# Kernel tuning notes

Hardware: AMD Instinct MI355X
Metric: run time of the kernel (lower is better)

## Reference

```python
import jax, jax.numpy as jnp
import numpy as np

N_HEAD = 16

def setup_inputs() -> dict:
    key = jax.random.key(0)
    ks = jax.random.split(key, 9)
    H = 2048
    def w(k, shape, scale=0.02):
        return jax.random.normal(k, shape, dtype=jnp.float32) * scale
    return {
        'h':  jax.random.normal(ks[0], (4, 2048, H), dtype=jnp.float32),
        'Wq': w(ks[1], (H, H)), 'bq': w(ks[2], (H,)),
        'Wk': w(ks[3], (H, H)), 'bk': w(ks[4], (H,)),
        'Wv': w(ks[5], (H, H)), 'bv': w(ks[6], (H,)),
        'Wo': w(ks[7], (H, H)), 'bo': w(ks[8], (H,)),
    }

def reference(h, Wq, bq, Wk, bk, Wv, bv, Wo, bo):
    B, S, H = h.shape
    nh = N_HEAD
    hd = H // nh
    # QKV projections (torch Linear: x @ W.T + b)
    q = (h @ Wq.T + bq).reshape(B, S, nh, hd)
    k = (h @ Wk.T + bk).reshape(B, S, nh, hd)
    v = (h @ Wv.T + bv).reshape(B, S, nh, hd)
    scale = 1.0 / jnp.sqrt(jnp.float32(hd))
    # causal attention scores [B, nh, S, S]
    scores = jnp.einsum('bqhd,bkhd->bhqk', q, k) * scale
    causal = jnp.tril(jnp.ones((S, S), dtype=bool))
    scores = jnp.where(causal, scores, jnp.finfo(scores.dtype).min)
    attn = jax.nn.softmax(scores, axis=-1)
    o = jnp.einsum('bhqk,bkhd->bqhd', attn, v).reshape(B, S, H)
    return o @ Wo.T + bo
```

## Files before the change

kernel.cpp:

```cpp
#include <hip/hip_runtime.h>
#include <hip/hip_bf16.h>
#include <math.h>


using bf16x8 = __attribute__((ext_vector_type(8))) __bf16;
using f32x4  = __attribute__((ext_vector_type(4))) float;
using s16x8  = __attribute__((ext_vector_type(8))) short;

#define MFMA16(a, b, c) __builtin_amdgcn_mfma_f32_16x16x32_bf16((a), (b), (c), 0, 0, 0)

__device__ __forceinline__ unsigned short f2bf(float f) {
  unsigned u = __float_as_uint(f);
  u += 0x7FFFu + ((u >> 16) & 1u);
  return (unsigned short)(u >> 16);
}

__device__ __forceinline__ void gload16(const void* g, void* l) {
  __builtin_amdgcn_global_load_lds((const __attribute__((address_space(1))) void*)g,
                                   (__attribute__((address_space(3))) void*)l,
                                   16, 0, 0);
}

__global__ void cvt_kernel(const float* __restrict__ in, unsigned short* __restrict__ out, int n4) {
  int i = blockIdx.x * 256 + threadIdx.x;
  if (i >= n4) return;
  float4 v = ((const float4*)in)[i];
  ushort4 o;
  o.x = f2bf(v.x); o.y = f2bf(v.y); o.z = f2bf(v.z); o.w = f2bf(v.w);
  ((ushort4*)out)[i] = o;
}


#define GEMM_PRE()                                                             \
  const int tid = threadIdx.x;                                                 \
  const int wave = tid >> 6, lane = tid & 63;                                  \
  const int lo = lane & 15, hi = lane >> 4;                                    \
  const int wr = wave >> 2, wc = wave & 3;                                     \
  const int r4 = lane >> 2, s4 = lane & 3;                                     \
  const int scol = ((s4 ^ ((r4 >> 1) & 3)) << 3);                              \
  const unsigned short* aS[2]; const unsigned short* bS[2];                    \
  _Pragma("unroll")                                                            \
  for (int j = 0; j < 2; ++j) {                                                \
    aS[j] = A + (size_t)(m0 + (wave * 2 + j) * 16 + r4) * 2048 + scol;         \
    bS[j] = W + (size_t)(n0 + (wave * 2 + j) * 16 + r4) * 2048 + scol;         \
  }                                                                            \
  f32x4 acc[8][4] = {};

#define STAGE2(BUF, J)                                                         \
  do {                                                                         \
    gload16(aS[J], &lA[BUF][(wave * 2 + (J)) * 512]);                          \
    gload16(bS[J], &lB[BUF][(wave * 2 + (J)) * 512]);                          \
    aS[J] += 32; bS[J] += 32;                                                  \
  } while (0)

#define LDA4_(dst, MH, BUF)                                                    \
  do {                                                                         \
    _Pragma("unroll")                                                          \
    for (int im = 0; im < 4; ++im)                                             \
      dst[im] = *(const bf16x8*)&lA[BUF][(wr * 128 + (MH)*64 + im * 16 + lo) * 32 + \
                                         ((hi ^ ((lo >> 1) & 3)) << 3)];       \
  } while (0)

#define LDB4_(dst, BUF)                                                        \
  do {                                                                         \
    _Pragma("unroll")                                                          \
    for (int ni = 0; ni < 4; ++ni)                                             \
      dst[ni] = *(const bf16x8*)&lB[BUF][(wc * 64 + ni * 16 + lo) * 32 +       \
                                         ((hi ^ ((lo >> 1) & 3)) << 3)];       \
  } while (0)

#define MF16(MH, aF, bF)                                                       \
  do {                                                                         \
    __builtin_amdgcn_s_setprio(1);                                             \
    _Pragma("unroll")                                                          \
    for (int im = 0; im < 4; ++im)                                             \
      _Pragma("unroll")                                                        \
      for (int ni = 0; ni < 4; ++ni)                                           \
        acc[(MH)*4 + im][ni] = MFMA16(aF[im], bF[ni], acc[(MH)*4 + im][ni]);   \
    __builtin_amdgcn_s_setprio(0);                                             \
  } while (0)

#define BAR __builtin_amdgcn_s_barrier()
#define VMC(N) asm volatile("s_waitcnt vmcnt(" #N ")" ::: "memory")

#define TILE(RBUF, SBUF, COND, VN)                                             \
  do {                                                                         \
    bf16x8 aF[4], aG[4], bF[4];                                                \
    LDA4_(aF, 0, RBUF); LDB4_(bF, RBUF);                                       \
    if (COND) STAGE2(SBUF, 0);                                                 \
    BAR; MF16(0, aF, bF); BAR;                                                 \
    LDA4_(aG, 1, RBUF);                                                        \
    if (COND) STAGE2(SBUF, 1);                                                 \
    BAR; MF16(1, aG, bF); VMC(VN); BAR;                                        \
  } while (0)

#define GEMM_MAIN()                                                            \
  STAGE2(0, 0); STAGE2(0, 1); STAGE2(1, 0); STAGE2(1, 1);                      \
  STAGE2(2, 0); STAGE2(2, 1);                                                  \
  VMC(8); BAR;                                                                 \
  for (int u = 0; u < 15; ++u) {                                               \
    TILE(0, 3, true, 8); TILE(1, 0, true, 8);                                  \
    TILE(2, 1, true, 8); TILE(3, 2, true, 8);                                  \
  }                                                                            \
  TILE(0, 3, true, 8); TILE(1, 0, false, 4);                                   \
  TILE(2, 1, false, 0); TILE(3, 2, false, 0);

__global__ __launch_bounds__(512, 2)
void gemm_qkv(const unsigned short* __restrict__ A,
              const unsigned short* __restrict__ W,
              const float* __restrict__ bq, const float* __restrict__ bk,
              const float* __restrict__ bv,
              unsigned short* __restrict__ Q, unsigned short* __restrict__ Kq,
              unsigned short* __restrict__ V) {
  __shared__ unsigned short lA[4][256 * 32];
  __shared__ unsigned short lB[4][256 * 32];
  const int bid = blockIdx.x;
  const int sid = (bid & 7) * 96 + (bid >> 3);
  const int bm = sid / 24, bn = sid % 24;
  const int m0 = bm * 256, n0 = bn * 256;
  GEMM_PRE();
  GEMM_MAIN();

  const int which = n0 >> 11;
  const float* bias = (which == 0) ? bq : (which == 1) ? bk : bv;
  unsigned short* dst = (which == 0) ? Q : (which == 1) ? Kq : V;
#pragma unroll
  for (int mi = 0; mi < 8; mi++)
#pragma unroll
    for (int ni = 0; ni < 4; ni++) {
      int n_g = n0 + wc * 64 + ni * 16 + lo;
      int n2 = n_g & 2047;
      int head = n2 >> 7, d = n2 & 127;
      float bb = bias[n2];
#pragma unroll
      for (int i = 0; i < 4; i++) {
        int m = m0 + wr * 128 + mi * 16 + hi * 4 + i;
        int b = m >> 11, s = m & 2047;
        dst[(((size_t)b * 16 + head) * 2048 + s) * 128 + d] = f2bf(acc[mi][ni][i] + bb);
      }
    }
}

__global__ __launch_bounds__(512, 2)
void gemm_out(const unsigned short* __restrict__ A,
              const unsigned short* __restrict__ W,
              const float* __restrict__ bo, float* __restrict__ out) {
  __shared__ unsigned short lA[4][256 * 32];
  __shared__ unsigned short lB[4][256 * 32];
  const int bid = blockIdx.x;
  const int sid = (bid & 7) * 32 + (bid >> 3);
  const int bm = sid >> 3, bn = sid & 7;
  const int m0 = bm * 256, n0 = bn * 256;
  GEMM_PRE();
  GEMM_MAIN();

#pragma unroll
  for (int mi = 0; mi < 8; mi++)
#pragma unroll
    for (int ni = 0; ni < 4; ni++) {
      int n_g = n0 + wc * 64 + ni * 16 + lo;
      float bb = bo[n_g];
#pragma unroll
      for (int i = 0; i < 4; i++) {
        int m = m0 + wr * 128 + mi * 16 + hi * 4 + i;
        out[(size_t)m * 2048 + n_g] = acc[mi][ni][i] + bb;
      }
    }
}

__global__ __launch_bounds__(256, 2)
void attn_kernel(const unsigned short* __restrict__ Qb,
                 const unsigned short* __restrict__ Kb,
                 const unsigned short* __restrict__ Vb,
                 unsigned short* __restrict__ Ob) {
  __shared__ unsigned short lK[32 * 128];
  __shared__ unsigned short lVt[144 * 42];
  __shared__ unsigned short lP[4][32 * 40];

  const int tid = threadIdx.x;
  const int wave = tid >> 6, lane = tid & 63;
  const int lo = lane & 15, hi = lane >> 4;
  const int bh = blockIdx.x & 63;
  const int qt = 15 - (blockIdx.x >> 6);
  const int q0 = qt * 128 + wave * 32;
  const size_t base = (size_t)bh * 2048 * 128;
  const float SCL = 0.08838834764831845f * 1.4426950408889634f;
  const float THR = 11.5416f;

#pragma unroll
  for (int x = tid; x < 512; x += 256)
    lVt[(128 + (x >> 5)) * 42 + (x & 31)] = 0x3F80;

  bf16x8 aq[2][4];
#pragma unroll
  for (int mi = 0; mi < 2; mi++)
#pragma unroll
    for (int dk = 0; dk < 4; dk++)
      aq[mi][dk] = *(const bf16x8*)&Qb[base + (size_t)(q0 + mi * 16 + lo) * 128 + dk * 32 + hi * 8];

  f32x4 acc[2][9] = {};
  float mrun[2][4];
#pragma unroll
  for (int a = 0; a < 2; a++)
#pragma unroll
    for (int b = 0; b < 4; b++) mrun[a][b] = -INFINITY;

  const int ktn = qt * 4 + 4;
  const int qmax_w = q0 + 31;

  for (int kt = 0; kt < ktn; kt++) {
    __syncthreads();
#pragma unroll
    for (int j = 0; j < 2; j++) {
      int c = wave * 2 + j;
      int row = c * 4 + hi;
      int srccol = (lo * 16) ^ ((row & 7) << 4);
      const unsigned short* g = Kb + base + (size_t)(kt * 32 + row) * 128 + (srccol >> 1);
      gload16(g, &lK[c * 512]);
    }
    {
      int rr = tid & 15;
      int c0 = (tid >> 4) * 8;
      const unsigned short* vp = Vb + base + (size_t)(kt * 32 + 2 * rr) * 128 + c0;
      s16x8 va = *(const s16x8*)vp;
      s16x8 vb2 = *(const s16x8*)(vp + 128);
#pragma unroll
      for (int j = 0; j < 8; j++)
        *(ushort2*)&lVt[(c0 + j) * 42 + 2 * rr] =
            make_ushort2((unsigned short)va[j], (unsigned short)vb2[j]);
    }
    __syncthreads();

    if (kt * 32 <= qmax_w) {
      f32x4 sc[2][2] = {};
#pragma unroll
      for (int ni = 0; ni < 2; ni++)
#pragma unroll
        for (int dk = 0; dk < 4; dk++) {
          int row = ni * 16 + lo;
          int col = (dk * 32 + hi * 8) ^ ((row & 7) << 3);
          bf16x8 bk_ = *(const bf16x8*)&lK[row * 128 + col];
          sc[0][ni] = MFMA16(aq[0][dk], bk_, sc[0][ni]);
          sc[1][ni] = MFMA16(aq[1][dk], bk_, sc[1][ni]);
        }

      float s0_[2][4], s1_[2][4];
      bool cond = true;
#pragma unroll
      for (int mi = 0; mi < 2; mi++)
#pragma unroll
        for (int i = 0; i < 4; i++) {
          int qrow = q0 + mi * 16 + hi * 4 + i;
          int kc = kt * 32 + lo;
          float s0 = sc[mi][0][i] * SCL;
          float s1 = sc[mi][1][i] * SCL;
          if (kc > qrow) s0 = -INFINITY;
          if (kc + 16 > qrow) s1 = -INFINITY;
          s0_[mi][i] = s0; s1_[mi][i] = s1;
          cond = cond && (fmaxf(s0, s1) <= mrun[mi][i] + THR);
        }

      if (!__all((int)cond)) {
#pragma unroll
        for (int mi = 0; mi < 2; mi++)
#pragma unroll
          for (int i = 0; i < 4; i++) {
            float mt = fmaxf(s0_[mi][i], s1_[mi][i]);
            mt = fmaxf(mt, __shfl_xor(mt, 1));
            mt = fmaxf(mt, __shfl_xor(mt, 2));
            mt = fmaxf(mt, __shfl_xor(mt, 4));
            mt = fmaxf(mt, __shfl_xor(mt, 8));
            float mo = mrun[mi][i];
            float mn = fmaxf(mo, mt);
            float alpha = exp2f(mo - mn);
            mrun[mi][i] = mn;
#pragma unroll
            for (int ni = 0; ni < 9; ni++) acc[mi][ni][i] *= alpha;
          }
      }

      unsigned short* lPw = &lP[wave][0];
#pragma unroll
      for (int mi = 0; mi < 2; mi++)
#pragma unroll
        for (int i = 0; i < 4; i++) {
          float m = mrun[mi][i];
          float p0 = exp2f(s0_[mi][i] - m);
          float p1 = exp2f(s1_[mi][i] - m);
          int prow = mi * 16 + hi * 4 + i;
          lPw[prow * 40 + lo] = f2bf(p0);
          lPw[prow * 40 + 16 + lo] = f2bf(p1);
        }

      bf16x8 ap0 = *(const bf16x8*)&lPw[(lo) * 40 + hi * 8];
      bf16x8 ap1 = *(const bf16x8*)&lPw[(16 + lo) * 40 + hi * 8];
#pragma unroll
      for (int ni = 0; ni < 9; ni++) {
        bf16x8 bv_ = *(const bf16x8*)&lVt[(ni * 16 + lo) * 42 + hi * 8];
        acc[0][ni] = MFMA16(ap0, bv_, acc[0][ni]);
        acc[1][ni] = MFMA16(ap1, bv_, acc[1][ni]);
      }
    }
  }

  const int b = bh >> 4, hh = bh & 15;
#pragma unroll
  for (int mi = 0; mi < 2; mi++)
#pragma unroll
    for (int i = 0; i < 4; i++) {
      float inv = 1.0f / acc[mi][8][i];
      int s = q0 + mi * 16 + hi * 4 + i;
      size_t rowbase = ((size_t)b * 2048 + s) * 2048 + hh * 128 + lo;
#pragma unroll
      for (int ni = 0; ni < 8; ni++)
        Ob[rowbase + ni * 16] = f2bf(acc[mi][ni][i] * inv);
    }
}

extern "C" void kernel_launch(void* const* d_in, const int* in_sizes, int n_in,
                              void* d_out, int out_size, void* d_ws, size_t ws_size,
                              hipStream_t stream) {
  const float* h  = (const float*)d_in[0];
  const float* Wq = (const float*)d_in[1];
  const float* bq = (const float*)d_in[2];
  const float* Wk = (const float*)d_in[3];
  const float* bk = (const float*)d_in[4];
  const float* Wv = (const float*)d_in[5];
  const float* bv = (const float*)d_in[6];
  const float* Wo = (const float*)d_in[7];
  const float* bo = (const float*)d_in[8];
  float* out = (float*)d_out;

  char* ws = (char*)d_ws;
  unsigned short* h_bf  = (unsigned short*)(ws + 0);
  unsigned short* Qb    = (unsigned short*)(ws + 33554432);
  unsigned short* Kb    = (unsigned short*)(ws + 67108864);
  unsigned short* Vb    = (unsigned short*)(ws + 100663296);
  unsigned short* Wqkv  = (unsigned short*)(ws + 134217728);
  unsigned short* Wo_bf = (unsigned short*)(ws + 159383552);
  unsigned short* Ob    = h_bf;

  cvt_kernel<<<16384, 256, 0, stream>>>(h, h_bf, 4194304);
  cvt_kernel<<<4096, 256, 0, stream>>>(Wq, Wqkv, 1048576);
  cvt_kernel<<<4096, 256, 0, stream>>>(Wk, Wqkv + 4194304, 1048576);
  cvt_kernel<<<4096, 256, 0, stream>>>(Wv, Wqkv + 8388608, 1048576);
  cvt_kernel<<<4096, 256, 0, stream>>>(Wo, Wo_bf, 1048576);

  gemm_qkv<<<dim3(768), dim3(512), 0, stream>>>(h_bf, Wqkv, bq, bk, bv, Qb, Kb, Vb);

  attn_kernel<<<dim3(1024), dim3(256), 0, stream>>>(Qb, Kb, Vb, Ob);

  gemm_out<<<dim3(256), dim3(512), 0, stream>>>(Ob, Wo_bf, bo, out);
}
```

Before: 456.8 us.

## Double attention KV tile to 64 keys and drop mid-tile GEMM barriers

The attention kernel now processes 64 keys per iteration instead of 32, enlarging the K, transposed-V and P shared buffers and halving the loop trip count and the number of block-wide syncs. The QKV GEMM tile macro issues both staging loads up front and removes two of the four barriers per tile, so the two MFMA halves run back to back. The larger tiles raise LDS use and register pressure, which may reduce occupancy. Fewer barriers in the GEMM relies on the buffer rotation staying race-free.

Measured after the change: 455.1 us. About the same (-0.4%).

```diff
diff --git a/kernel.cpp b/kernel.cpp
--- a/kernel.cpp
+++ b/kernel.cpp
@@ -87,11 +87,12 @@
   do {                                                                         \
     bf16x8 aF[4], aG[4], bF[4];                                                \
     LDA4_(aF, 0, RBUF); LDB4_(bF, RBUF);                                       \
-    if (COND) STAGE2(SBUF, 0);                                                 \
-    BAR; MF16(0, aF, bF); BAR;                                                 \
+    if (COND) { STAGE2(SBUF, 0); STAGE2(SBUF, 1); }                            \
+    BAR;                                                                       \
+    MF16(0, aF, bF);                                                           \
     LDA4_(aG, 1, RBUF);                                                        \
-    if (COND) STAGE2(SBUF, 1);                                                 \
-    BAR; MF16(1, aG, bF); VMC(VN); BAR;                                        \
+    MF16(1, aG, bF);                                                           \
+    VMC(VN); BAR;                                                              \
   } while (0)
 
 #define GEMM_MAIN()                                                            \
@@ -173,9 +174,9 @@
                  const unsigned short* __restrict__ Kb,
                  const unsigned short* __restrict__ Vb,
                  unsigned short* __restrict__ Ob) {
-  __shared__ unsigned short lK[32 * 128];
-  __shared__ unsigned short lVt[144 * 42];
-  __shared__ unsigned short lP[4][32 * 40];
+  __shared__ unsigned short lK[64 * 128];
+  __shared__ unsigned short lVt[144 * 72];
+  __shared__ unsigned short lP[4][32 * 72];
 
   const int tid = threadIdx.x;
   const int wave = tid >> 6, lane = tid & 63;
@@ -188,8 +189,8 @@
   const float THR = 11.5416f;
 
 #pragma unroll
-  for (int x = tid; x < 512; x += 256)
-    lVt[(128 + (x >> 5)) * 42 + (x & 31)] = 0x3F80;
+  for (int x = tid; x < 1024; x += 256)
+    lVt[(128 + (x >> 6)) * 72 + (x & 63)] = 0x3F80;
 
   bf16x8 aq[2][4];
 #pragma unroll
@@ -205,36 +206,39 @@
 #pragma unroll
     for (int b = 0; b < 4; b++) mrun[a][b] = -INFINITY;
 
-  const int ktn = qt * 4 + 4;
+  const int ktn = qt * 2 + 2;
   const int qmax_w = q0 + 31;
 
   for (int kt = 0; kt < ktn; kt++) {
     __syncthreads();
 #pragma unroll
-    for (int j = 0; j < 2; j++) {
-      int c = wave * 2 + j;
-      int row = c * 4 + hi;
-      int srccol = (lo * 16) ^ ((row & 7) << 4);
-      const unsigned short* g = Kb + base + (size_t)(kt * 32 + row) * 128 + (srccol >> 1);
-      gload16(g, &lK[c * 512]);
+    for (int j = 0; j < 4; j++) {
+      int lrow = j * 16 + wave * 4 + hi;
+      int srccol = (lo * 16) ^ ((lrow & 7) << 4);
+      gload16(Kb + base + (size_t)(kt * 64 + lrow) * 128 + (srccol >> 1),
+              &lK[(j * 16 + wave * 4) * 128]);
     }
     {
-      int rr = tid & 15;
-      int c0 = (tid >> 4) * 8;
-      const unsigned short* vp = Vb + base + (size_t)(kt * 32 + 2 * rr) * 128 + c0;
-      s16x8 va = *(const s16x8*)vp;
-      s16x8 vb2 = *(const s16x8*)(vp + 128);
-#pragma unroll
-      for (int j = 0; j < 8; j++)
-        *(ushort2*)&lVt[(c0 + j) * 42 + 2 * rr] =
-            make_ushort2((unsigned short)va[j], (unsigned short)vb2[j]);
+      int rr = tid & 31;
+      int c0 = (tid >> 5) * 8;
+#pragma unroll
+      for (int half = 0; half < 2; half++) {
+        int cc = c0 + half * 64;
+        const unsigned short* vp = Vb + base + (size_t)(kt * 64 + 2 * rr) * 128 + cc;
+        s16x8 va = *(const s16x8*)vp;
+        s16x8 vb2 = *(const s16x8*)(vp + 128);
+#pragma unroll
+        for (int j = 0; j < 8; j++)
+          *(ushort2*)&lVt[(cc + j) * 72 + 2 * rr] =
+              make_ushort2((unsigned short)va[j], (unsigned short)vb2[j]);
+      }
     }
     __syncthreads();
 
-    if (kt * 32 <= qmax_w) {
-      f32x4 sc[2][2] = {};
-#pragma unroll
-      for (int ni = 0; ni < 2; ni++)
+    if (kt * 64 <= qmax_w) {
+      f32x4 sc[2][4] = {};
+#pragma unroll
+      for (int ni = 0; ni < 4; ni++)
 #pragma unroll
         for (int dk = 0; dk < 4; dk++) {
           int row = ni * 16 + lo;
@@ -244,20 +248,24 @@
           sc[1][ni] = MFMA16(aq[1][dk], bk_, sc[1][ni]);
         }
 
-      float s0_[2][4], s1_[2][4];
+      float tm[2][4];
       bool cond = true;
 #pragma unroll
       for (int mi = 0; mi < 2; mi++)
 #pragma unroll
         for (int i = 0; i < 4; i++) {
           int qrow = q0 + mi * 16 + hi * 4 + i;
-          int kc = kt * 32 + lo;
-          float s0 = sc[mi][0][i] * SCL;
-          float s1 = sc[mi][1][i] * SCL;
-          if (kc > qrow) s0 = -INFINITY;
-          if (kc + 16 > qrow) s1 = -INFINITY;
-          s0_[mi][i] = s0; s1_[mi][i] = s1;
-          cond = cond && (fmaxf(s0, s1) <= mrun[mi][i] + THR);
+          float mx = -INFINITY;
+#pragma unroll
+          for (int ni = 0; ni < 4; ni++) {
+            int kc = kt * 64 + ni * 16 + lo;
+            float s = sc[mi][ni][i] * SCL;
+            if (kc > qrow) s = -INFINITY;
+            sc[mi][ni][i] = s;
+            mx = fmaxf(mx, s);
+          }
+          tm[mi][i] = mx;
+          cond = cond && (mx <= mrun[mi][i] + THR);
         }
 
       if (!__all((int)cond)) {
@@ -265,7 +273,7 @@
         for (int mi = 0; mi < 2; mi++)
 #pragma unroll
           for (int i = 0; i < 4; i++) {
-            float mt = fmaxf(s0_[mi][i], s1_[mi][i]);
+            float mt = tm[mi][i];
             mt = fmaxf(mt, __shfl_xor(mt, 1));
             mt = fmaxf(mt, __shfl_xor(mt, 2));
             mt = fmaxf(mt, __shfl_xor(mt, 4));
@@ -285,21 +293,26 @@
 #pragma unroll
         for (int i = 0; i < 4; i++) {
           float m = mrun[mi][i];
-          float p0 = exp2f(s0_[mi][i] - m);
-          float p1 = exp2f(s1_[mi][i] - m);
           int prow = mi * 16 + hi * 4 + i;
-          lPw[prow * 40 + lo] = f2bf(p0);
-          lPw[prow * 40 + 16 + lo] = f2bf(p1);
+#pragma unroll
+          for (int ni = 0; ni < 4; ni++)
+            lPw[prow * 72 + ni * 16 + lo] = f2bf(exp2f(sc[mi][ni][i] - m));
         }
 
-      bf16x8 ap0 = *(const bf16x8*)&lPw[(lo) * 40 + hi * 8];
-      bf16x8 ap1 = *(const bf16x8*)&lPw[(16 + lo) * 40 + hi * 8];
-#pragma unroll
-      for (int ni = 0; ni < 9; ni++) {
-        bf16x8 bv_ = *(const bf16x8*)&lVt[(ni * 16 + lo) * 42 + hi * 8];
-        acc[0][ni] = MFMA16(ap0, bv_, acc[0][ni]);
-        acc[1][ni] = MFMA16(ap1, bv_, acc[1][ni]);
-      }
+      bf16x8 ap[2][2];
+#pragma unroll
+      for (int mi = 0; mi < 2; mi++)
+#pragma unroll
+        for (int k2 = 0; k2 < 2; k2++)
+          ap[mi][k2] = *(const bf16x8*)&lPw[(mi * 16 + lo) * 72 + k2 * 32 + hi * 8];
+#pragma unroll
+      for (int ni = 0; ni < 9; ni++)
+#pragma unroll
+        for (int k2 = 0; k2 < 2; k2++) {
+          bf16x8 bv_ = *(const bf16x8*)&lVt[(ni * 16 + lo) * 72 + k2 * 32 + hi * 8];
+          acc[0][ni] = MFMA16(ap[0][k2], bv_, acc[0][ni]);
+          acc[1][ni] = MFMA16(ap[1][k2], bv_, acc[1][ni]);
+        }
     }
   }
 
```
